# Optimization experiments

Hardware: AMD Instinct MI355X
Metric: run time of the kernel (lower is better)

The kernel has to match this reference:

```python
import jax, jax.numpy as jnp
import numpy as np


def _segsum(x):
    """x: (..., T) -> (..., T, T) with [i,j] = sum_{k=j+1..i} x[k] for i>=j else -inf."""
    T = x.shape[-1]
    i = jnp.arange(T)
    strict_lower = i[:, None] > i[None, :]
    xx = jnp.where(strict_lower, x[..., :, None], 0.0)
    s = jnp.cumsum(xx, axis=-2)
    return jnp.where(i[:, None] >= i[None, :], s, -jnp.inf)


def setup_inputs() -> dict:
    key = jax.random.key(0)
    kX, kA, kB, kC = jax.random.split(key, 4)
    b, S, h, p, n = 8, 4096, 16, 64, 64
    X = jax.random.normal(kX, (b, S, h, p), jnp.float32)
    # decay-like A (negative) keeps exp(cumsum) finite at seq 4096; same math as module
    A = -jnp.abs(jax.random.normal(kA, (b, S, h), jnp.float32)) * 0.1
    B = jax.random.normal(kB, (b, S, h, n), jnp.float32)
    C = jax.random.normal(kC, (b, S, h, n), jnp.float32)
    initial_states = jnp.zeros((b, 1, h, p, n), jnp.float32)
    return {"X": X, "initial_states": initial_states, "A": A, "B": B, "C": C, "chunk_size": 64}


def reference(X, initial_states, A, B, C, chunk_size):
    b, S, h, p = X.shape
    n = B.shape[-1]
    c = S // chunk_size
    l = chunk_size
    # chunk: b (c l) ... -> b c l ...
    Xc = X.reshape(b, c, l, h, p)
    Bc = B.reshape(b, c, l, h, n)
    Cc = C.reshape(b, c, l, h, n)
    Ac = A.reshape(b, c, l, h).transpose(0, 3, 1, 2)  # b h c l
    A_cumsum = jnp.cumsum(Ac, axis=-1)                 # b h c l
    # 1. intra-chunk (diagonal) output
    Lm = jnp.exp(_segsum(Ac))                          # b h c l l
    Y_diag = jnp.einsum('bclhn,bcshn,bhcls,bcshp->bclhp', Cc, Bc, Lm, Xc)
    # 2. per-chunk states
    decay_states = jnp.exp(A_cumsum[..., -1:] - A_cumsum)  # b h c l
    states = jnp.einsum('bclhn,bhcl,bclhp->bchpn', Bc, decay_states, Xc)
    # 3. inter-chunk recurrence (via chunk-level segsum)
    states = jnp.concatenate([initial_states, states], axis=1)  # b (c+1) h p n
    A_last = jnp.pad(A_cumsum[..., -1], ((0, 0), (0, 0), (1, 0)))  # b h (c+1)
    decay_chunk = jnp.exp(_segsum(A_last))                         # b h (c+1) (c+1)
    new_states = jnp.einsum('bhzc,bchpn->bzhpn', decay_chunk, states)
    states = new_states[:, :-1]  # b c h p n (final_state = new_states[:, -1], unused)
    # 4. state -> output
    state_decay_out = jnp.exp(A_cumsum)  # b h c l
    Y_off = jnp.einsum('bclhn,bchpn,bhcl->bclhp', Cc, states, state_decay_out)
    return (Y_diag + Y_off).reshape(b, S, h, p)
```

## Files before the change

### kernel.cpp

```cpp
#include <hip/hip_runtime.h>


typedef __bf16 bf16x4 __attribute__((ext_vector_type(4)));
typedef __bf16 bf16x8 __attribute__((ext_vector_type(8)));
typedef float  f32x4  __attribute__((ext_vector_type(4)));

constexpr int LDT = 72;

__device__ __forceinline__ f32x4 mfma16(bf16x8 a, bf16x8 b, f32x4 c) {
    return __builtin_amdgcn_mfma_f32_16x16x32_bf16(a, b, c, 0, 0, 0);
}
__device__ __forceinline__ void bar_lds() {
    asm volatile("s_waitcnt lgkmcnt(0)\n\ts_barrier" ::: "memory");
}
__device__ __forceinline__ int swz(int row, int byteoff) {
    return byteoff ^ (((row >> 2) & 7) << 4);
}

struct SMemF {
    __bf16 Cm[64][LDT];
    __bf16 Bm[64][LDT];
    __bf16 Bt[64][LDT];
    __bf16 Mm[64][LDT];
    __bf16 Xt[2][32][LDT];
    __bf16 St16[32][LDT];
    float  St32[32][68];
    float  sY[64][36];
    float  ds[3][64];
    float  dout[3][64];
    float  douti[3][64];
    float  dlast[3];
};

__global__ void ssd_fused(const float* __restrict__ Xg, const float* __restrict__ Ig,
                          const float* __restrict__ Ag, const float* __restrict__ Bg,
                          const float* __restrict__ Cg, float* __restrict__ Yg)
{
    const int ph = blockIdx.x, hh = blockIdx.y, bb = blockIdx.z;
    const int tid = threadIdx.x;
    const int wid = tid >> 6, lane = tid & 63;
    const int fr = lane & 15, fg = lane >> 4;
    const int iw2 = (wid >> 1) * 16;
    const int pt  = (wid & 1) * 16;
    const int jh  = (wid & 1) * 32;

    __shared__ __align__(16) SMemF sm;
    const size_t tbase = (size_t)bb * 4096;

    const int half = tid >> 8;
    const int u    = tid & 255;
    const int lt0  = (u >> 4) * 4;
    const int rr0  = u >> 4;
    const int cq0  = (u & 15) * 4;
    const int xl  = tid >> 3;
    const int xp4 = (tid & 7) * 4;
    const int sp  = tid >> 4;
    const int sn4 = (tid & 15) * 4;

    float rb[4][4], rx[4];
    float aA = 0.0f;

    {
        const size_t iofs = (((size_t)bb*16 + hh)*64 + (ph*32 + sp))*(size_t)64 + sn4;
        const float4 v = *reinterpret_cast<const float4*>(&Ig[iofs]);
        sm.St32[sp][sn4+0] = v.x; sm.St32[sp][sn4+1] = v.y;
        sm.St32[sp][sn4+2] = v.z; sm.St32[sp][sn4+3] = v.w;
        *reinterpret_cast<bf16x4*>(&sm.St16[sp][sn4]) =
            (bf16x4){(__bf16)v.x, (__bf16)v.y, (__bf16)v.z, (__bf16)v.w};
    }
    #pragma unroll
    for (int j = 0; j < 4; ++j) {
        const int row = (half == 0) ? (lt0 + j) : (rr0 + 16*j);
        const size_t go = ((tbase + row)*16 + hh)*(size_t)64 + cq0;
        *reinterpret_cast<float4*>(rb[j]) = (half == 0)
            ? *reinterpret_cast<const float4*>(&Bg[go])
            : *reinterpret_cast<const float4*>(&Cg[go]);
    }
    *reinterpret_cast<float4*>(rx) =
        *reinterpret_cast<const float4*>(&Xg[((tbase + xl)*16 + hh)*(size_t)64 + ph*32 + xp4]);
    if (wid == 0) aA = Ag[(tbase + lane)*16 + hh];

    if (wid == 0) {
        float v = aA;
        #pragma unroll
        for (int o = 1; o < 64; o <<= 1) { float t = __shfl_up(v, o, 64); if (lane >= o) v += t; }
        const float last = __shfl(v, 63, 64);
        sm.ds[0][lane]    = expf(last - v);
        sm.dout[0][lane]  = expf(v);
        sm.douti[0][lane] = expf(v - last);
        if (lane == 63) sm.dlast[0] = expf(v);
    }
    if (half == 0) {
        #pragma unroll
        for (int j = 0; j < 4; ++j)
            *reinterpret_cast<bf16x4*>(&sm.Bm[lt0 + j][cq0]) =
                (bf16x4){(__bf16)rb[j][0], (__bf16)rb[j][1], (__bf16)rb[j][2], (__bf16)rb[j][3]};
        #pragma unroll
        for (int q = 0; q < 4; ++q)
            *reinterpret_cast<bf16x4*>(
                reinterpret_cast<char*>(&sm.Bt[cq0 + q][0]) + swz(cq0 + q, lt0*2)) =
                (bf16x4){(__bf16)rb[0][q], (__bf16)rb[1][q], (__bf16)rb[2][q], (__bf16)rb[3][q]};
    } else {
        #pragma unroll
        for (int j = 0; j < 4; ++j)
            *reinterpret_cast<bf16x4*>(&sm.Cm[rr0 + 16*j][cq0]) =
                (bf16x4){(__bf16)rb[j][0], (__bf16)rb[j][1], (__bf16)rb[j][2], (__bf16)rb[j][3]};
    }
    bar_lds();
    {
        const float dsl = sm.ds[0][xl];
        #pragma unroll
        for (int q = 0; q < 4; ++q)
            *reinterpret_cast<__bf16*>(
                reinterpret_cast<char*>(&sm.Xt[0][xp4 + q][0]) + swz(xp4 + q, xl*2)) =
                (__bf16)(rx[q] * dsl);
    }
    #pragma unroll
    for (int j = 0; j < 4; ++j) {
        const int row = (half == 0) ? (lt0 + j) : (rr0 + 16*j);
        const size_t go = ((tbase + 64 + row)*16 + hh)*(size_t)64 + cq0;
        *reinterpret_cast<float4*>(rb[j]) = (half == 0)
            ? *reinterpret_cast<const float4*>(&Bg[go])
            : *reinterpret_cast<const float4*>(&Cg[go]);
    }
    *reinterpret_cast<float4*>(rx) =
        *reinterpret_cast<const float4*>(&Xg[((tbase + 64 + xl)*16 + hh)*(size_t)64 + ph*32 + xp4]);
    if (wid == 0) aA = Ag[(tbase + 64 + lane)*16 + hh];
    bar_lds();

    f32x4 aoprev = {};
    int t0 = 0, t1 = 1, t2 = 2;

    for (int c = 0; c < 64; ++c) {
        const int ci = c & 1, nb = ci ^ 1;

        f32x4 g0 = {}, g1 = {}, aoacc = {}, stacc = {};
        #pragma unroll
        for (int ks = 0; ks < 2; ++ks) {
            const int k0 = ks*32 + fg*8;
            const bf16x8 aC  = *reinterpret_cast<const bf16x8*>(&sm.Cm[iw2 + fr][k0]);
            const bf16x8 bB0 = *reinterpret_cast<const bf16x8*>(&sm.Bm[jh      + fr][k0]);
            const bf16x8 bB1 = *reinterpret_cast<const bf16x8*>(&sm.Bm[jh + 16 + fr][k0]);
            const bf16x8 bSt = *reinterpret_cast<const bf16x8*>(&sm.St16[pt + fr][k0]);
            const bf16x8 aBt = *reinterpret_cast<const bf16x8*>(
                reinterpret_cast<const char*>(&sm.Bt[iw2 + fr][0]) + swz(iw2 + fr, k0*2));
            const bf16x8 bXt = *reinterpret_cast<const bf16x8*>(
                reinterpret_cast<const char*>(&sm.Xt[ci][pt + fr][0]) + swz(pt + fr, k0*2));
            g0    = mfma16(aC,  bB0, g0);
            g1    = mfma16(aC,  bB1, g1);
            aoacc = mfma16(aC,  bSt, aoacc);
            stacc = mfma16(aBt, bXt, stacc);
        }
        if (c > 0) {
            f32x4 ad = {};
            #pragma unroll
            for (int ks = 0; ks < 2; ++ks) {
                const int k0 = ks*32 + fg*8;
                const bf16x8 aM = *reinterpret_cast<const bf16x8*>(&sm.Mm[iw2 + fr][k0]);
                const bf16x8 bX = *reinterpret_cast<const bf16x8*>(
                    reinterpret_cast<const char*>(&sm.Xt[nb][pt + fr][0]) + swz(pt + fr, k0*2));
                ad = mfma16(aM, bX, ad);
            }
            #pragma unroll
            for (int r = 0; r < 4; ++r) {
                const int i = iw2 + fg*4 + r;
                sm.sY[i][pt + fr] = ad[r] + sm.dout[t2][i] * aoprev[r];
            }
        }
        if (c < 63 && wid == 0) {
            float v = aA;
            #pragma unroll
            for (int o = 1; o < 64; o <<= 1) { float t = __shfl_up(v, o, 64); if (lane >= o) v += t; }
            const float last = __shfl(v, 63, 64);
            sm.ds[t1][lane]    = expf(last - v);
            sm.dout[t1][lane]  = expf(v);
            sm.douti[t1][lane] = expf(v - last);
            if (lane == 63) sm.dlast[t1] = expf(v);
        }
        aoprev = aoacc;
        bar_lds();

        if (c > 0) {
            const float4 v = *reinterpret_cast<const float4*>(&sm.sY[xl][xp4]);
            *reinterpret_cast<float4*>(
                &Yg[((tbase + (size_t)(c-1)*64 + xl)*16 + hh)*(size_t)64 + ph*32 + xp4]) = v;
        }
        {
            #pragma unroll
            for (int jt = 0; jt < 2; ++jt) {
                const int j = jh + jt*16 + fr;
                const f32x4& gg = jt ? g1 : g0;
                #pragma unroll
                for (int r = 0; r < 4; ++r) {
                    const int i = iw2 + fg*4 + r;
                    const float val = (i >= j) ? gg[r] * sm.douti[t0][i] : 0.0f;
                    sm.Mm[i][j] = (__bf16)val;
                }
            }
        }
        {
            const float dl = sm.dlast[t0];
            const int p = pt + fr, n0 = iw2 + fg*4;
            const float4 ov = *reinterpret_cast<const float4*>(&sm.St32[p][n0]);
            float4 nv;
            nv.x = fmaf(dl, ov.x, stacc[0]); nv.y = fmaf(dl, ov.y, stacc[1]);
            nv.z = fmaf(dl, ov.z, stacc[2]); nv.w = fmaf(dl, ov.w, stacc[3]);
            *reinterpret_cast<float4*>(&sm.St32[p][n0]) = nv;
            *reinterpret_cast<bf16x4*>(&sm.St16[p][n0]) =
                (bf16x4){(__bf16)nv.x, (__bf16)nv.y, (__bf16)nv.z, (__bf16)nv.w};
        }
        if (c < 63) {
            if (half == 0) {
                #pragma unroll
                for (int j = 0; j < 4; ++j)
                    *reinterpret_cast<bf16x4*>(&sm.Bm[lt0 + j][cq0]) =
                        (bf16x4){(__bf16)rb[j][0], (__bf16)rb[j][1], (__bf16)rb[j][2], (__bf16)rb[j][3]};
                #pragma unroll
                for (int q = 0; q < 4; ++q)
                    *reinterpret_cast<bf16x4*>(
                        reinterpret_cast<char*>(&sm.Bt[cq0 + q][0]) + swz(cq0 + q, lt0*2)) =
                        (bf16x4){(__bf16)rb[0][q], (__bf16)rb[1][q], (__bf16)rb[2][q], (__bf16)rb[3][q]};
            } else {
                #pragma unroll
                for (int j = 0; j < 4; ++j)
                    *reinterpret_cast<bf16x4*>(&sm.Cm[rr0 + 16*j][cq0]) =
                        (bf16x4){(__bf16)rb[j][0], (__bf16)rb[j][1], (__bf16)rb[j][2], (__bf16)rb[j][3]};
            }
            const float dsl = sm.ds[t1][xl];
            #pragma unroll
            for (int q = 0; q < 4; ++q)
                *reinterpret_cast<__bf16*>(
                    reinterpret_cast<char*>(&sm.Xt[nb][xp4 + q][0]) + swz(xp4 + q, xl*2)) =
                    (__bf16)(rx[q] * dsl);
        }
        if (c < 62) {
            const size_t s2 = tbase + (size_t)(c + 2)*64;
            #pragma unroll
            for (int j = 0; j < 4; ++j) {
                const int row = (half == 0) ? (lt0 + j) : (rr0 + 16*j);
                const size_t go = ((s2 + row)*16 + hh)*(size_t)64 + cq0;
                *reinterpret_cast<float4*>(rb[j]) = (half == 0)
                    ? *reinterpret_cast<const float4*>(&Bg[go])
                    : *reinterpret_cast<const float4*>(&Cg[go]);
            }
            *reinterpret_cast<float4*>(rx) =
                *reinterpret_cast<const float4*>(&Xg[((s2 + xl)*16 + hh)*(size_t)64 + ph*32 + xp4]);
            if (wid == 0) aA = Ag[(s2 + lane)*16 + hh];
        }
        bar_lds();

        const int tt = t0; t0 = t1; t1 = t2; t2 = tt;
    }

    {
        f32x4 ad = {};
        #pragma unroll
        for (int ks = 0; ks < 2; ++ks) {
            const int k0 = ks*32 + fg*8;
            const bf16x8 aM = *reinterpret_cast<const bf16x8*>(&sm.Mm[iw2 + fr][k0]);
            const bf16x8 bX = *reinterpret_cast<const bf16x8*>(
                reinterpret_cast<const char*>(&sm.Xt[1][pt + fr][0]) + swz(pt + fr, k0*2));
            ad = mfma16(aM, bX, ad);
        }
        #pragma unroll
        for (int r = 0; r < 4; ++r) {
            const int i = iw2 + fg*4 + r;
            sm.sY[i][pt + fr] = ad[r] + sm.dout[t2][i] * aoprev[r];
        }
    }
    bar_lds();
    {
        const float4 v = *reinterpret_cast<const float4*>(&sm.sY[xl][xp4]);
        *reinterpret_cast<float4*>(
            &Yg[((tbase + (size_t)63*64 + xl)*16 + hh)*(size_t)64 + ph*32 + xp4]) = v;
    }
}

extern "C" void kernel_launch(void* const* d_in, const int* in_sizes, int n_in,
                              void* d_out, int out_size, void* d_ws, size_t ws_size,
                              hipStream_t stream) {
    const float* X  = (const float*)d_in[0];
    const float* I  = (const float*)d_in[1];
    const float* A  = (const float*)d_in[2];
    const float* Bp = (const float*)d_in[3];
    const float* Cp = (const float*)d_in[4];
    float* Y = (float*)d_out;
    ssd_fused<<<dim3(2, 16, 8), 512, 0, stream>>>(X, I, A, Bp, Cp, Y);
}
```

Baseline: 146.1 us.

## Double-buffer LDS tiles to cut per-chunk barriers from two to one

Double-buffers the C, B, Bt, M, state and output tiles in LDS, gives Xt three buffers, and rotates the decay tables through four slots, so each chunk iteration needs a single barrier instead of two. The output store, the decay scan and the next-chunk staging move ahead of the M and state updates, and the A prefetch reaches one chunk further ahead. This is meant to remove barrier stalls and overlap global stores and loads with MFMA work. In exchange LDS use roughly doubles, which may lower occupancy, and the buffer-index bookkeeping becomes more complex.

```diff
diff --git a/kernel.cpp b/kernel.cpp
--- a/kernel.cpp
+++ b/kernel.cpp
@@ -18,18 +18,18 @@
 }
 
 struct SMemF {
-    __bf16 Cm[64][LDT];
-    __bf16 Bm[64][LDT];
-    __bf16 Bt[64][LDT];
-    __bf16 Mm[64][LDT];
-    __bf16 Xt[2][32][LDT];
-    __bf16 St16[32][LDT];
+    __bf16 Cm[2][64][LDT];
+    __bf16 Bm[2][64][LDT];
+    __bf16 Bt[2][64][LDT];
+    __bf16 Mm[2][64][LDT];
+    __bf16 Xt[3][32][LDT];
+    __bf16 St16[2][32][LDT];
     float  St32[32][68];
-    float  sY[64][36];
-    float  ds[3][64];
-    float  dout[3][64];
-    float  douti[3][64];
-    float  dlast[3];
+    float  sY[2][64][36];
+    float  ds[4][64];
+    float  dout[4][64];
+    float  douti[4][64];
+    float  dlast[4];
 };
 
 __global__ void ssd_fused(const float* __restrict__ Xg, const float* __restrict__ Ig,
@@ -60,12 +60,22 @@
     float rb[4][4], rx[4];
     float aA = 0.0f;
 
+    auto scan_to = [&](float v, int tb) {
+        #pragma unroll
+        for (int o = 1; o < 64; o <<= 1) { float t = __shfl_up(v, o, 64); if (lane >= o) v += t; }
+        const float last = __shfl(v, 63, 64);
+        sm.ds[tb][lane]    = expf(last - v);
+        sm.dout[tb][lane]  = expf(v);
+        sm.douti[tb][lane] = expf(v - last);
+        if (lane == 63) sm.dlast[tb] = expf(v);
+    };
+
     {
         const size_t iofs = (((size_t)bb*16 + hh)*64 + (ph*32 + sp))*(size_t)64 + sn4;
         const float4 v = *reinterpret_cast<const float4*>(&Ig[iofs]);
         sm.St32[sp][sn4+0] = v.x; sm.St32[sp][sn4+1] = v.y;
         sm.St32[sp][sn4+2] = v.z; sm.St32[sp][sn4+3] = v.w;
-        *reinterpret_cast<bf16x4*>(&sm.St16[sp][sn4]) =
+        *reinterpret_cast<bf16x4*>(&sm.St16[0][sp][sn4]) =
             (bf16x4){(__bf16)v.x, (__bf16)v.y, (__bf16)v.z, (__bf16)v.w};
     }
     #pragma unroll
@@ -78,32 +88,24 @@
     }
     *reinterpret_cast<float4*>(rx) =
         *reinterpret_cast<const float4*>(&Xg[((tbase + xl)*16 + hh)*(size_t)64 + ph*32 + xp4]);
-    if (wid == 0) aA = Ag[(tbase + lane)*16 + hh];
-
-    if (wid == 0) {
-        float v = aA;
-        #pragma unroll
-        for (int o = 1; o < 64; o <<= 1) { float t = __shfl_up(v, o, 64); if (lane >= o) v += t; }
-        const float last = __shfl(v, 63, 64);
-        sm.ds[0][lane]    = expf(last - v);
-        sm.dout[0][lane]  = expf(v);
-        sm.douti[0][lane] = expf(v - last);
-        if (lane == 63) sm.dlast[0] = expf(v);
+    if (wid < 2) {
+        const float v = Ag[(tbase + wid*64 + lane)*16 + hh];
+        scan_to(v, wid);
     }
     if (half == 0) {
         #pragma unroll
         for (int j = 0; j < 4; ++j)
-            *reinterpret_cast<bf16x4*>(&sm.Bm[lt0 + j][cq0]) =
+            *reinterpret_cast<bf16x4*>(&sm.Bm[0][lt0 + j][cq0]) =
                 (bf16x4){(__bf16)rb[j][0], (__bf16)rb[j][1], (__bf16)rb[j][2], (__bf16)rb[j][3]};
         #pragma unroll
         for (int q = 0; q < 4; ++q)
             *reinterpret_cast<bf16x4*>(
-                reinterpret_cast<char*>(&sm.Bt[cq0 + q][0]) + swz(cq0 + q, lt0*2)) =
+                reinterpret_cast<char*>(&sm.Bt[0][cq0 + q][0]) + swz(cq0 + q, lt0*2)) =
                 (bf16x4){(__bf16)rb[0][q], (__bf16)rb[1][q], (__bf16)rb[2][q], (__bf16)rb[3][q]};
     } else {
         #pragma unroll
         for (int j = 0; j < 4; ++j)
-            *reinterpret_cast<bf16x4*>(&sm.Cm[rr0 + 16*j][cq0]) =
+            *reinterpret_cast<bf16x4*>(&sm.Cm[0][rr0 + 16*j][cq0]) =
                 (bf16x4){(__bf16)rb[j][0], (__bf16)rb[j][1], (__bf16)rb[j][2], (__bf16)rb[j][3]};
     }
     bar_lds();
@@ -125,80 +127,107 @@
     }
     *reinterpret_cast<float4*>(rx) =
         *reinterpret_cast<const float4*>(&Xg[((tbase + 64 + xl)*16 + hh)*(size_t)64 + ph*32 + xp4]);
-    if (wid == 0) aA = Ag[(tbase + 64 + lane)*16 + hh];
+    if (wid == 0) aA = Ag[(tbase + 2*64 + lane)*16 + hh];
     bar_lds();
 
     f32x4 aoprev = {};
-    int t0 = 0, t1 = 1, t2 = 2;
+    int x0 = 0, x1 = 1, x2 = 2;
 
     for (int c = 0; c < 64; ++c) {
         const int ci = c & 1, nb = ci ^ 1;
+        const int t0 = c & 3, t1 = (c+1) & 3, t2 = (c+2) & 3, t3 = (c+3) & 3;
 
         f32x4 g0 = {}, g1 = {}, aoacc = {}, stacc = {};
         #pragma unroll
         for (int ks = 0; ks < 2; ++ks) {
             const int k0 = ks*32 + fg*8;
-            const bf16x8 aC  = *reinterpret_cast<const bf16x8*>(&sm.Cm[iw2 + fr][k0]);
-            const bf16x8 bB0 = *reinterpret_cast<const bf16x8*>(&sm.Bm[jh      + fr][k0]);
-            const bf16x8 bB1 = *reinterpret_cast<const bf16x8*>(&sm.Bm[jh + 16 + fr][k0]);
-            const bf16x8 bSt = *reinterpret_cast<const bf16x8*>(&sm.St16[pt + fr][k0]);
+            const bf16x8 aC  = *reinterpret_cast<const bf16x8*>(&sm.Cm[ci][iw2 + fr][k0]);
+            const bf16x8 bB0 = *reinterpret_cast<const bf16x8*>(&sm.Bm[ci][jh      + fr][k0]);
+            const bf16x8 bB1 = *reinterpret_cast<const bf16x8*>(&sm.Bm[ci][jh + 16 + fr][k0]);
+            const bf16x8 bSt = *reinterpret_cast<const bf16x8*>(&sm.St16[ci][pt + fr][k0]);
             const bf16x8 aBt = *reinterpret_cast<const bf16x8*>(
-                reinterpret_cast<const char*>(&sm.Bt[iw2 + fr][0]) + swz(iw2 + fr, k0*2));
+                reinterpret_cast<const char*>(&sm.Bt[ci][iw2 + fr][0]) + swz(iw2 + fr, k0*2));
             const bf16x8 bXt = *reinterpret_cast<const bf16x8*>(
-                reinterpret_cast<const char*>(&sm.Xt[ci][pt + fr][0]) + swz(pt + fr, k0*2));
+                reinterpret_cast<const char*>(&sm.Xt[x0][pt + fr][0]) + swz(pt + fr, k0*2));
             g0    = mfma16(aC,  bB0, g0);
             g1    = mfma16(aC,  bB1, g1);
             aoacc = mfma16(aC,  bSt, aoacc);
             stacc = mfma16(aBt, bXt, stacc);
         }
+        f32x4 ad = {};
         if (c > 0) {
-            f32x4 ad = {};
             #pragma unroll
             for (int ks = 0; ks < 2; ++ks) {
                 const int k0 = ks*32 + fg*8;
-                const bf16x8 aM = *reinterpret_cast<const bf16x8*>(&sm.Mm[iw2 + fr][k0]);
+                const bf16x8 aM = *reinterpret_cast<const bf16x8*>(&sm.Mm[nb][iw2 + fr][k0]);
                 const bf16x8 bX = *reinterpret_cast<const bf16x8*>(
-                    reinterpret_cast<const char*>(&sm.Xt[nb][pt + fr][0]) + swz(pt + fr, k0*2));
+                    reinterpret_cast<const char*>(&sm.Xt[x2][pt + fr][0]) + swz(pt + fr, k0*2));
                 ad = mfma16(aM, bX, ad);
             }
+        }
+        if (c <= 61 && wid == 0) scan_to(aA, t2);
+        if (c >= 2) {
+            const float4 v = *reinterpret_cast<const float4*>(&sm.sY[nb][xl][xp4]);
+            *reinterpret_cast<float4*>(
+                &Yg[((tbase + (size_t)(c-2)*64 + xl)*16 + hh)*(size_t)64 + ph*32 + xp4]) = v;
+        }
+        if (c < 63) {
+            if (half == 0) {
+                #pragma unroll
+                for (int j = 0; j < 4; ++j)
+                    *reinterpret_cast<bf16x4*>(&sm.Bm[nb][lt0 + j][cq0]) =
+                        (bf16x4){(__bf16)rb[j][0], (__bf16)rb[j][1], (__bf16)rb[j][2], (__bf16)rb[j][3]};
+                #pragma unroll
+                for (int q = 0; q < 4; ++q)
+                    *reinterpret_cast<bf16x4*>(
+                        reinterpret_cast<char*>(&sm.Bt[nb][cq0 + q][0]) + swz(cq0 + q, lt0*2)) =
+                        (bf16x4){(__bf16)rb[0][q], (__bf16)rb[1][q], (__bf16)rb[2][q], (__bf16)rb[3][q]};
+            } else {
+                #pragma unroll
+                for (int j = 0; j < 4; ++j)
+                    *reinterpret_cast<bf16x4*>(&sm.Cm[nb][rr0 + 16*j][cq0]) =
+                        (bf16x4){(__bf16)rb[j][0], (__bf16)rb[j][1], (__bf16)rb[j][2], (__bf16)rb[j][3]};
+            }
+            const float dsl = sm.ds[t1][xl];
+            #pragma unroll
+            for (int q = 0; q < 4; ++q)
+                *reinterpret_cast<__bf16*>(
+                    reinterpret_cast<char*>(&sm.Xt[x1][xp4 + q][0]) + swz(xp4 + q, xl*2)) =
+                    (__bf16)(rx[q] * dsl);
+        }
+        if (c < 62) {
+            const size_t s2 = tbase + (size_t)(c + 2)*64;
+            #pragma unroll
+            for (int j = 0; j < 4; ++j) {
+                const int row = (half == 0) ? (lt0 + j) : (rr0 + 16*j);
+                const size_t go = ((s2 + row)*16 + hh)*(size_t)64 + cq0;
+                *reinterpret_cast<float4*>(rb[j]) = (half == 0)
+                    ? *reinterpret_cast<const float4*>(&Bg[go])
+                    : *reinterpret_cast<const float4*>(&Cg[go]);
+            }
+            *reinterpret_cast<float4*>(rx) =
+                *reinterpret_cast<const float4*>(&Xg[((s2 + xl)*16 + hh)*(size_t)64 + ph*32 + xp4]);
+        }
+        if (wid == 0 && c <= 60) aA = Ag[(tbase + (size_t)(c + 3)*64 + lane)*16 + hh];
+        if (c > 0) {
             #pragma unroll
             for (int r = 0; r < 4; ++r) {
                 const int i = iw2 + fg*4 + r;
-                sm.sY[i][pt + fr] = ad[r] + sm.dout[t2][i] * aoprev[r];
-            }
-        }
-        if (c < 63 && wid == 0) {
-            float v = aA;
-            #pragma unroll
-            for (int o = 1; o < 64; o <<= 1) { float t = __shfl_up(v, o, 64); if (lane >= o) v += t; }
-            const float last = __shfl(v, 63, 64);
-            sm.ds[t1][lane]    = expf(last - v);
-            sm.dout[t1][lane]  = expf(v);
-            sm.douti[t1][lane] = expf(v - last);
-            if (lane == 63) sm.dlast[t1] = expf(v);
-        }
-        aoprev = aoacc;
-        bar_lds();
-
-        if (c > 0) {
-            const float4 v = *reinterpret_cast<const float4*>(&sm.sY[xl][xp4]);
-            *reinterpret_cast<float4*>(
-                &Yg[((tbase + (size_t)(c-1)*64 + xl)*16 + hh)*(size_t)64 + ph*32 + xp4]) = v;
-        }
-        {
-            #pragma unroll
-            for (int jt = 0; jt < 2; ++jt) {
-                const int j = jh + jt*16 + fr;
-                const f32x4& gg = jt ? g1 : g0;
-                #pragma unroll
-                for (int r = 0; r < 4; ++r) {
-                    const int i = iw2 + fg*4 + r;
-                    const float val = (i >= j) ? gg[r] * sm.douti[t0][i] : 0.0f;
-                    sm.Mm[i][j] = (__bf16)val;
-                }
-            }
-        }
-        {
+                sm.sY[ci][i][pt + fr] = ad[r] + sm.dout[t3][i] * aoprev[r];
+            }
+        }
+        #pragma unroll
+        for (int jt = 0; jt < 2; ++jt) {
+            const int j = jh + jt*16 + fr;
+            const f32x4& gg = jt ? g1 : g0;
+            #pragma unroll
+            for (int r = 0; r < 4; ++r) {
+                const int i = iw2 + fg*4 + r;
+                const float val = (i >= j) ? gg[r] * sm.douti[t0][i] : 0.0f;
+                sm.Mm[ci][i][j] = (__bf16)val;
+            }
+        }
+        if (c < 63) {
             const float dl = sm.dlast[t0];
             const int p = pt + fr, n0 = iw2 + fg*4;
             const float4 ov = *reinterpret_cast<const float4*>(&sm.St32[p][n0]);
@@ -206,50 +235,12 @@
             nv.x = fmaf(dl, ov.x, stacc[0]); nv.y = fmaf(dl, ov.y, stacc[1]);
             nv.z = fmaf(dl, ov.z, stacc[2]); nv.w = fmaf(dl, ov.w, stacc[3]);
             *reinterpret_cast<float4*>(&sm.St32[p][n0]) = nv;
-            *reinterpret_cast<bf16x4*>(&sm.St16[p][n0]) =
+            *reinterpret_cast<bf16x4*>(&sm.St16[nb][p][n0]) =
                 (bf16x4){(__bf16)nv.x, (__bf16)nv.y, (__bf16)nv.z, (__bf16)nv.w};
         }
-        if (c < 63) {
-            if (half == 0) {
-                #pragma unroll
-                for (int j = 0; j < 4; ++j)
-                    *reinterpret_cast<bf16x4*>(&sm.Bm[lt0 + j][cq0]) =
-                        (bf16x4){(__bf16)rb[j][0], (__bf16)rb[j][1], (__bf16)rb[j][2], (__bf16)rb[j][3]};
-                #pragma unroll
-                for (int q = 0; q < 4; ++q)
-                    *reinterpret_cast<bf16x4*>(
-                        reinterpret_cast<char*>(&sm.Bt[cq0 + q][0]) + swz(cq0 + q, lt0*2)) =
-                        (bf16x4){(__bf16)rb[0][q], (__bf16)rb[1][q], (__bf16)rb[2][q], (__bf16)rb[3][q]};
-            } else {
-                #pragma unroll
-                for (int j = 0; j < 4; ++j)
-                    *reinterpret_cast<bf16x4*>(&sm.Cm[rr0 + 16*j][cq0]) =
-                        (bf16x4){(__bf16)rb[j][0], (__bf16)rb[j][1], (__bf16)rb[j][2], (__bf16)rb[j][3]};
-            }
-            const float dsl = sm.ds[t1][xl];
-            #pragma unroll
-            for (int q = 0; q < 4; ++q)
-                *reinterpret_cast<__bf16*>(
-                    reinterpret_cast<char*>(&sm.Xt[nb][xp4 + q][0]) + swz(xp4 + q, xl*2)) =
-                    (__bf16)(rx[q] * dsl);
-        }
-        if (c < 62) {
-            const size_t s2 = tbase + (size_t)(c + 2)*64;
-            #pragma unroll
-            for (int j = 0; j < 4; ++j) {
-                const int row = (half == 0) ? (lt0 + j) : (rr0 + 16*j);
-                const size_t go = ((s2 + row)*16 + hh)*(size_t)64 + cq0;
-                *reinterpret_cast<float4*>(rb[j]) = (half == 0)
-                    ? *reinterpret_cast<const float4*>(&Bg[go])
-                    : *reinterpret_cast<const float4*>(&Cg[go]);
-            }
-            *reinterpret_cast<float4*>(rx) =
-                *reinterpret_cast<const float4*>(&Xg[((s2 + xl)*16 + hh)*(size_t)64 + ph*32 + xp4]);
-            if (wid == 0) aA = Ag[(s2 + lane)*16 + hh];
-        }
+        aoprev = aoacc;
         bar_lds();
-
-        const int tt = t0; t0 = t1; t1 = t2; t2 = tt;
+        const int xt = x0; x0 = x1; x1 = x2; x2 = xt;
     }
 
     {
@@ -257,20 +248,25 @@
         #pragma unroll
         for (int ks = 0; ks < 2; ++ks) {
             const int k0 = ks*32 + fg*8;
-            const bf16x8 aM = *reinterpret_cast<const bf16x8*>(&sm.Mm[iw2 + fr][k0]);
+            const bf16x8 aM = *reinterpret_cast<const bf16x8*>(&sm.Mm[1][iw2 + fr][k0]);
             const bf16x8 bX = *reinterpret_cast<const bf16x8*>(
-                reinterpret_cast<const char*>(&sm.Xt[1][pt + fr][0]) + swz(pt + fr, k0*2));
+                reinterpret_cast<const char*>(&sm.Xt[x2][pt + fr][0]) + swz(pt + fr, k0*2));
             ad = mfma16(aM, bX, ad);
         }
         #pragma unroll
         for (int r = 0; r < 4; ++r) {
             const int i = iw2 + fg*4 + r;
-            sm.sY[i][pt + fr] = ad[r] + sm.dout[t2][i] * aoprev[r];
-        }
+            sm.sY[0][i][pt + fr] = ad[r] + sm.dout[3][i] * aoprev[r];
+        }
+    }
+    {
+        const float4 v = *reinterpret_cast<const float4*>(&sm.sY[1][xl][xp4]);
+        *reinterpret_cast<float4*>(
+            &Yg[((tbase + (size_t)62*64 + xl)*16 + hh)*(size_t)64 + ph*32 + xp4]) = v;
     }
     bar_lds();
     {
-        const float4 v = *reinterpret_cast<const float4*>(&sm.sY[xl][xp4]);
+        const float4 v = *reinterpret_cast<const float4*>(&sm.sY[0][xl][xp4]);
         *reinterpret_cast<float4*>(
             &Yg[((tbase + (size_t)63*64 + xl)*16 + hh)*(size_t)64 + ph*32 + xp4]) = v;
     }
```

Result: faster. 132.8 us, median of 2 (-9.1%).
